# Performance work log

Hardware: AMD Instinct MI355X
Metric: run time of the kernel (lower is better)

## Reference

```python
import jax, jax.numpy as jnp
import numpy as np

D_MODEL = 1024
D_FF = 4096
N_EXPERTS = 4
D_HID = D_MODEL // 2
TOP_K = 2
B, T = 2, 4096


def setup_inputs() -> dict:
    key = jax.random.key(0)
    ks = jax.random.split(key, 10)
    s_in = 1.0 / np.sqrt(D_MODEL)
    s_ff = 1.0 / np.sqrt(D_FF)
    s_h = 1.0 / np.sqrt(D_HID)
    return {
        "x": jax.random.normal(ks[0], (B, T, D_MODEL), jnp.float32),
        # stacked expert FFN params [E, ...]
        "w1": jax.random.normal(ks[1], (N_EXPERTS, D_MODEL, D_FF), jnp.float32) * s_in,
        "b1": jnp.zeros((N_EXPERTS, D_FF), jnp.float32),
        "w2": jax.random.normal(ks[2], (N_EXPERTS, D_FF, D_MODEL), jnp.float32) * s_ff,
        "b2": jnp.zeros((N_EXPERTS, D_MODEL), jnp.float32),
        # router MLP params
        "wr1": jax.random.normal(ks[3], (D_MODEL, D_HID), jnp.float32) * s_in,
        "br1": jnp.zeros((D_HID,), jnp.float32),
        "wr2": jax.random.normal(ks[4], (D_HID, N_EXPERTS), jnp.float32) * s_h,
        "br2": jnp.zeros((N_EXPERTS,), jnp.float32),
    }


def _gelu(x):
    return jax.nn.gelu(x, approximate=False)  # torch nn.GELU default is exact erf


def reference(x, w1, b1, w2, b2, wr1, br1, wr2, br2):
    # Router: 2-layer MLP -> logits [B,T,E]
    h = _gelu(jnp.einsum('btd,dh->bth', x, wr1) + br1)
    logits = jnp.einsum('bth,he->bte', h, wr2) + br2
    # top-k masked softmax over experts
    top_vals, _ = jax.lax.top_k(logits, TOP_K)
    thresh = top_vals[..., -1:]
    masked = jnp.where(logits >= thresh, logits, -jnp.inf)
    gate = jax.nn.softmax(masked, axis=-1)  # [B,T,E], zeros off top-k
    # dense all-experts FFN: hid [B,T,E,d_ff]
    hid = _gelu(jnp.einsum('btd,edf->btef', x, w1) + b1)
    expert_outs = jnp.einsum('btef,efd->bted', hid, w2) + b2  # [B,T,E,d_model]
    out = jnp.einsum('bte,bted->btd', gate, expert_outs)
    return out, gate
```

## Files before the change

kernel.cpp:

```cpp
#include <hip/hip_runtime.h>

#define NTOK 8192
#define DM 1024
#define DF 4096
#define DH 512
#define NE 4
#define SLOTS (NTOK * 2)

typedef unsigned short ushort_t;
typedef short bf16x8 __attribute__((ext_vector_type(8)));
typedef float f32x4 __attribute__((ext_vector_type(4)));

__device__ __forceinline__ unsigned short f2bf(float f) {
    unsigned int u = __float_as_uint(f);
    u += 0x7FFFu + ((u >> 16) & 1u);
    return (unsigned short)(u >> 16);
}
__device__ __forceinline__ float bf2f(unsigned short h) {
    return __uint_as_float(((unsigned int)h) << 16);
}
__device__ __forceinline__ float gelu_exact(float x) {
    return 0.5f * x * (1.0f + erff(x * 0.7071067811865476f));
}
__device__ __forceinline__ float gelu_fast(float x) {
    float u = 1.5957691216057308f * (x + 0.044715f * x * x * x);
    return x / (1.0f + __expf(-u));
}
__device__ __forceinline__ void gload16(const void* g, void* l) {
    __builtin_amdgcn_global_load_lds((__attribute__((address_space(1))) void*)(g),
                                     (__attribute__((address_space(3))) void*)(l), 16, 0, 0);
}
__device__ __forceinline__ int swz(int b) { return b ^ (((b >> 7) & 3) << 4); }
__device__ __forceinline__ int imin(int a, int b) { return a < b ? a : b; }

__global__ __launch_bounds__(256) void k_cast_split(const float* __restrict__ in,
                                                    ushort_t* __restrict__ hi,
                                                    ushort_t* __restrict__ lo, int n4) {
    int i = blockIdx.x * 256 + threadIdx.x;
    if (i >= n4) return;
    float4 v = ((const float4*)in)[i];
    ushort4 h, l;
    h.x = f2bf(v.x); l.x = f2bf(v.x - bf2f(h.x));
    h.y = f2bf(v.y); l.y = f2bf(v.y - bf2f(h.y));
    h.z = f2bf(v.z); l.z = f2bf(v.z - bf2f(h.z));
    h.w = f2bf(v.w); l.w = f2bf(v.w - bf2f(h.w));
    ((ushort4*)hi)[i] = h;
    ((ushort4*)lo)[i] = l;
}

template <bool SPLIT>
__global__ __launch_bounds__(256) void k_tcast(const float* __restrict__ in,
                                               ushort_t* __restrict__ oh,
                                               ushort_t* __restrict__ ol, int K, int N) {
    __shared__ float t[64][65];
    size_t base = (size_t)blockIdx.z * K * N;
    const float* src = in + base;
    int k0 = blockIdx.y * 64, n0 = blockIdx.x * 64;
    int tx = threadIdx.x & 63, ty = threadIdx.x >> 6;
#pragma unroll
    for (int i = 0; i < 16; i++) {
        int r = ty + i * 4;
        t[r][tx] = src[(size_t)(k0 + r) * N + n0 + tx];
    }
    __syncthreads();
#pragma unroll
    for (int i = 0; i < 16; i++) {
        int nn = ty + i * 4;
        float v = t[tx][nn];
        unsigned short hv = f2bf(v);
        size_t o = base + (size_t)(n0 + nn) * K + k0 + tx;
        oh[o] = hv;
        if (SPLIT) ol[o] = f2bf(v - bf2f(hv));
    }
}

template <int MODE>
__global__ __launch_bounds__(256) void k_gemm(
    const ushort_t* __restrict__ A0, const ushort_t* __restrict__ B0,
    const ushort_t* __restrict__ A1, const ushort_t* __restrict__ B1,
    const ushort_t* __restrict__ A2, const ushort_t* __restrict__ B2,
    int K, int N,
    const float* __restrict__ bias, const float* __restrict__ gate,
    const int* __restrict__ idx, const int4* __restrict__ tiles,
    const int* __restrict__ meta,
    float* __restrict__ outF, ushort_t* __restrict__ ghid, float* __restrict__ outA)
{
    int e = 0, rstart = 0, rows = 128, gbase = 0;
    if (MODE != 0) {
        if ((int)blockIdx.y >= meta[0]) return;
        int4 ti = tiles[blockIdx.y];
        e = ti.x; rstart = ti.y; rows = ti.z; gbase = ti.w;
    }
    __shared__ ushort_t lA[4096];
    __shared__ ushort_t lB[4096];
    int row0 = (MODE == 0) ? blockIdx.y * 128 : 0;
    int col0 = blockIdx.x * 128;
    int tid = threadIdx.x, lane = tid & 63, wv = tid >> 6;
    int wr = wv >> 1, wc = wv & 1;
    int r15 = lane & 15, hq = lane >> 4;

    f32x4 z = {0.f, 0.f, 0.f, 0.f};
    f32x4 acc[4][4];
#pragma unroll
    for (int m = 0; m < 4; m++)
#pragma unroll
        for (int n = 0; n < 4; n++) acc[m][n] = z;

    int d0 = tid * 16, d1 = d0 + 4096;
    int u0 = swz(d0), u1 = swz(d1);
    int rA0 = u0 >> 6, ko0 = ((u0 >> 4) & 3) * 8;
    int rA1 = u1 >> 6, ko1 = ((u1 >> 4) & 3) * 8;
    char* ldA0 = (char*)lA + wv * 1024;
    char* ldA1 = (char*)lA + 4096 + wv * 1024;
    char* ldB0 = (char*)lB + wv * 1024;
    char* ldB1 = (char*)lB + 4096 + wv * 1024;

    auto compute = [&]() {
        bf16x8 af[4], bfr[4];
#pragma unroll
        for (int m = 0; m < 4; m++) {
            int u = ((wr * 64 + m * 16 + r15) << 6) + (hq << 4);
            af[m] = *(const bf16x8*)((const char*)lA + swz(u));
        }
#pragma unroll
        for (int n = 0; n < 4; n++) {
            int u = ((wc * 64 + n * 16 + r15) << 6) + (hq << 4);
            bfr[n] = *(const bf16x8*)((const char*)lB + swz(u));
        }
#pragma unroll
        for (int m = 0; m < 4; m++)
#pragma unroll
            for (int n = 0; n < 4; n++)
                acc[m][n] = __builtin_amdgcn_mfma_f32_16x16x32_bf16(af[m], bfr[n], acc[m][n], 0, 0, 0);
    };

    if (MODE == 0) {
#pragma unroll
        for (int p = 0; p < 3; p++) {
            const ushort_t* A = (p == 0) ? A0 : ((p == 1) ? A1 : A2);
            const ushort_t* B = (p == 0) ? B0 : ((p == 1) ? B1 : B2);
            const ushort_t* Ab0 = A + (size_t)(row0 + rA0) * K + ko0;
            const ushort_t* Ab1 = A + (size_t)(row0 + rA1) * K + ko1;
            const ushort_t* Bb0 = B + (size_t)(col0 + rA0) * K + ko0;
            const ushort_t* Bb1 = B + (size_t)(col0 + rA1) * K + ko1;
            for (int kt = 0; kt < K; kt += 32) {
                gload16(Ab0 + kt, ldA0);
                gload16(Ab1 + kt, ldA1);
                gload16(Bb0 + kt, ldB0);
                gload16(Bb1 + kt, ldB1);
                __syncthreads();
                compute();
                __syncthreads();
            }
        }
    } else {
        const ushort_t *Ab0, *Ab1, *Bb0, *Bb1;
        if (MODE == 1) {
            int t0 = idx[e * NTOK + rstart + imin(rA0, rows - 1)];
            int t1 = idx[e * NTOK + rstart + imin(rA1, rows - 1)];
            Ab0 = A0 + (size_t)t0 * K + ko0;
            Ab1 = A0 + (size_t)t1 * K + ko1;
            Bb0 = B0 + ((size_t)e * DF + col0 + rA0) * K + ko0;
            Bb1 = B0 + ((size_t)e * DF + col0 + rA1) * K + ko1;
        } else {
            Ab0 = A0 + (size_t)(gbase + imin(rA0, rows - 1)) * K + ko0;
            Ab1 = A0 + (size_t)(gbase + imin(rA1, rows - 1)) * K + ko1;
            Bb0 = B0 + ((size_t)e * DM + col0 + rA0) * K + ko0;
            Bb1 = B0 + ((size_t)e * DM + col0 + rA1) * K + ko1;
        }
        for (int kt = 0; kt < K; kt += 32) {
            gload16(Ab0 + kt, ldA0);
            gload16(Ab1 + kt, ldA1);
            gload16(Bb0 + kt, ldB0);
            gload16(Bb1 + kt, ldB1);
            __syncthreads();
            compute();
            __syncthreads();
        }
    }

    if (MODE == 0) {
#pragma unroll
        for (int m = 0; m < 4; m++)
#pragma unroll
            for (int q = 0; q < 4; q++) {
                int row = row0 + wr * 64 + m * 16 + hq * 4 + q;
#pragma unroll
                for (int n = 0; n < 4; n++) {
                    int col = col0 + wc * 64 + n * 16 + r15;
                    outF[(size_t)row * N + col] = gelu_exact(acc[m][n][q] + bias[col]);
                }
            }
    } else if (MODE == 1) {
#pragma unroll
        for (int m = 0; m < 4; m++)
#pragma unroll
            for (int q = 0; q < 4; q++) {
                int lr = wr * 64 + m * 16 + hq * 4 + q;
                if (lr < rows) {
                    int token = idx[e * NTOK + rstart + lr];
                    float g = gate[token * 4 + e];
                    size_t rb = (size_t)(gbase + lr) * N;
#pragma unroll
                    for (int n = 0; n < 4; n++) {
                        int col = col0 + wc * 64 + n * 16 + r15;
                        float v = gelu_fast(acc[m][n][q] + bias[(size_t)e * N + col]) * g;
                        ghid[rb + col] = f2bf(v);
                    }
                }
            }
    } else {
#pragma unroll
        for (int m = 0; m < 4; m++)
#pragma unroll
            for (int q = 0; q < 4; q++) {
                int lr = wr * 64 + m * 16 + hq * 4 + q;
                if (lr < rows) {
                    int token = idx[e * NTOK + rstart + lr];
#pragma unroll
                    for (int n = 0; n < 4; n++) {
                        int col = col0 + wc * 64 + n * 16 + r15;
                        atomicAdd(&outA[(size_t)token * N + col], acc[m][n][q]);
                    }
                }
            }
    }
}

__global__ __launch_bounds__(256) void k_gate(const float* __restrict__ h,
                                              const float* __restrict__ wr2,
                                              const float* __restrict__ br2,
                                              float* __restrict__ gate,
                                              int* __restrict__ cnt,
                                              int* __restrict__ idx) {
    int t = blockIdx.x * 4 + (threadIdx.x >> 6);
    int lane = threadIdx.x & 63;
    const float* hr = h + (size_t)t * DH;
    const float4* w4 = (const float4*)wr2;
    float gx = 0.f, gy = 0.f, gz = 0.f, gw = 0.f;
#pragma unroll
    for (int j = 0; j < 8; j++) {
        int k = lane * 8 + j;
        float hv = hr[k];
        float4 w = w4[k];
        gx += hv * w.x; gy += hv * w.y; gz += hv * w.z; gw += hv * w.w;
    }
#pragma unroll
    for (int off = 32; off > 0; off >>= 1) {
        gx += __shfl_xor(gx, off);
        gy += __shfl_xor(gy, off);
        gz += __shfl_xor(gz, off);
        gw += __shfl_xor(gw, off);
    }
    if (lane == 0) {
        float ls[4];
        ls[0] = gx + br2[0]; ls[1] = gy + br2[1]; ls[2] = gz + br2[2]; ls[3] = gw + br2[3];
        int i1 = 0; float m1 = ls[0];
#pragma unroll
        for (int i = 1; i < 4; i++) if (ls[i] > m1) { m1 = ls[i]; i1 = i; }
        int i2 = -1; float m2 = -1e30f;
#pragma unroll
        for (int i = 0; i < 4; i++) if (i != i1 && ls[i] > m2) { m2 = ls[i]; i2 = i; }
        float e0 = (ls[0] >= m2) ? expf(ls[0] - m1) : 0.f;
        float e1 = (ls[1] >= m2) ? expf(ls[1] - m1) : 0.f;
        float e2 = (ls[2] >= m2) ? expf(ls[2] - m1) : 0.f;
        float e3 = (ls[3] >= m2) ? expf(ls[3] - m1) : 0.f;
        float iz = 1.f / (e0 + e1 + e2 + e3);
        float4 g = {e0 * iz, e1 * iz, e2 * iz, e3 * iz};
        ((float4*)gate)[t] = g;
        int s0 = atomicAdd(&cnt[i1], 1);
        idx[i1 * NTOK + s0] = t;
        int s1 = atomicAdd(&cnt[i2], 1);
        idx[i2 * NTOK + s1] = t;
    }
}

__global__ void k_tiles(const int* __restrict__ cnt, int4* __restrict__ tiles,
                        int* __restrict__ meta) {
    if (threadIdx.x != 0 || blockIdx.x != 0) return;
    int base = 0, nt = 0;
    for (int e = 0; e < NE; e++) {
        int c = cnt[e];
        for (int r = 0; r < c; r += 128) {
            int4 ti;
            ti.x = e; ti.y = r; ti.z = (c - r < 128) ? (c - r) : 128; ti.w = base + r;
            tiles[nt++] = ti;
        }
        base += c;
    }
    meta[0] = nt;
}

__global__ __launch_bounds__(256) void k_init_out(const float* __restrict__ gate,
                                                  const float* __restrict__ b2,
                                                  float* __restrict__ out) {
    int i = blockIdx.x * 256 + threadIdx.x;
    int t = i >> 8;
    int c4 = i & 255;
    float4 g = ((const float4*)gate)[t];
    const float4* b = (const float4*)b2;
    float4 v0 = b[c4], v1 = b[256 + c4], v2 = b[512 + c4], v3 = b[768 + c4];
    float4 o;
    o.x = g.x * v0.x + g.y * v1.x + g.z * v2.x + g.w * v3.x;
    o.y = g.x * v0.y + g.y * v1.y + g.z * v2.y + g.w * v3.y;
    o.z = g.x * v0.z + g.y * v1.z + g.z * v2.z + g.w * v3.z;
    o.w = g.x * v0.w + g.y * v1.w + g.z * v2.w + g.w * v3.w;
    ((float4*)out)[i] = o;
}

extern "C" void kernel_launch(void* const* d_in, const int* in_sizes, int n_in,
                              void* d_out, int out_size, void* d_ws, size_t ws_size,
                              hipStream_t stream) {
    const float* x   = (const float*)d_in[0];
    const float* w1  = (const float*)d_in[1];
    const float* b1  = (const float*)d_in[2];
    const float* w2  = (const float*)d_in[3];
    const float* b2  = (const float*)d_in[4];
    const float* wr1 = (const float*)d_in[5];
    const float* br1 = (const float*)d_in[6];
    const float* wr2 = (const float*)d_in[7];
    const float* br2 = (const float*)d_in[8];
    float* out  = (float*)d_out;
    float* gate = out + (size_t)NTOK * DM;

    char* p = (char*)d_ws;
    auto take = [&](size_t bytes) { char* r = p; p += (bytes + 255) & ~(size_t)255; return r; };
    ushort_t* xh    = (ushort_t*)take((size_t)NTOK * DM * 2);
    ushort_t* w1T   = (ushort_t*)take((size_t)NE * DF * DM * 2);
    ushort_t* w2T   = (ushort_t*)take((size_t)NE * DM * DF * 2);
    ushort_t* wr1Th = (ushort_t*)take((size_t)DH * DM * 2);
    ushort_t* wr1Tl = (ushort_t*)take((size_t)DH * DM * 2);
    int*      cnt   = (int*)take(64);
    int*      idx   = (int*)take((size_t)NE * NTOK * 4);
    int4*     tiles = (int4*)take(144 * 16);
    int*      meta  = (int*)take(64);
    char*     region = take((size_t)SLOTS * DF * 2);
    ushort_t* xl    = (ushort_t*)region;
    float*    h     = (float*)(region + (size_t)NTOK * DM * 2);
    ushort_t* ghid  = (ushort_t*)region;

    hipMemsetAsync(cnt, 0, 64, stream);

    k_cast_split<<<NTOK * DM / 4 / 256, 256, 0, stream>>>(x, xh, xl, NTOK * DM / 4);
    k_tcast<false><<<dim3(DF / 64, DM / 64, NE), 256, 0, stream>>>(w1, w1T, nullptr, DM, DF);
    k_tcast<false><<<dim3(DM / 64, DF / 64, NE), 256, 0, stream>>>(w2, w2T, nullptr, DF, DM);
    k_tcast<true ><<<dim3(DH / 64, DM / 64, 1),  256, 0, stream>>>(wr1, wr1Th, wr1Tl, DM, DH);

    k_gemm<0><<<dim3(DH / 128, NTOK / 128), 256, 0, stream>>>(
        xh, wr1Th, xh, wr1Tl, xl, wr1Th, DM, DH, br1,
        nullptr, nullptr, nullptr, nullptr, h, nullptr, nullptr);
    k_gate<<<NTOK / 4, 256, 0, stream>>>(h, wr2, br2, gate, cnt, idx);
    k_tiles<<<1, 64, 0, stream>>>(cnt, tiles, meta);
    k_init_out<<<NTOK * DM / 4 / 256, 256, 0, stream>>>(gate, b2, out);

    k_gemm<1><<<dim3(DF / 128, 132), 256, 0, stream>>>(
        xh, w1T, nullptr, nullptr, nullptr, nullptr, DM, DF, b1,
        gate, idx, tiles, meta, nullptr, ghid, nullptr);
    k_gemm<2><<<dim3(DM / 128, 132), 256, 0, stream>>>(
        ghid, w2T, nullptr, nullptr, nullptr, nullptr, DF, DM, nullptr,
        nullptr, idx, tiles, meta, nullptr, nullptr, out);
}
```

Before: 967.8 us.

## Double-buffer expert GEMMs with 128x256 tiles and XCD-aware block remapping

Splits the router GEMM into its own kernel. The expert GEMMs now use 512-thread blocks with 128x256 output tiles and double-buffered LDS staging, so the next k-slice loads while the current one computes and one barrier per k-step is dropped. It also adds a 1D grid with block-ID remapping across the 8 XCDs for L2 locality. The trade-offs are more LDS per block (48KB) and higher register pressure under launch_bounds(512,4), which could lower occupancy.

```diff
diff --git a/kernel.cpp b/kernel.cpp
--- a/kernel.cpp
+++ b/kernel.cpp
@@ -6,6 +6,7 @@
 #define DH 512
 #define NE 4
 #define SLOTS (NTOK * 2)
+#define NYT_MAX 132
 
 typedef unsigned short ushort_t;
 typedef short bf16x8 __attribute__((ext_vector_type(8)));
@@ -74,27 +75,15 @@
     }
 }
 
-template <int MODE>
-__global__ __launch_bounds__(256) void k_gemm(
+__global__ __launch_bounds__(256) void k_rgemm(
     const ushort_t* __restrict__ A0, const ushort_t* __restrict__ B0,
     const ushort_t* __restrict__ A1, const ushort_t* __restrict__ B1,
     const ushort_t* __restrict__ A2, const ushort_t* __restrict__ B2,
-    int K, int N,
-    const float* __restrict__ bias, const float* __restrict__ gate,
-    const int* __restrict__ idx, const int4* __restrict__ tiles,
-    const int* __restrict__ meta,
-    float* __restrict__ outF, ushort_t* __restrict__ ghid, float* __restrict__ outA)
+    int K, int N, const float* __restrict__ bias, float* __restrict__ outF)
 {
-    int e = 0, rstart = 0, rows = 128, gbase = 0;
-    if (MODE != 0) {
-        if ((int)blockIdx.y >= meta[0]) return;
-        int4 ti = tiles[blockIdx.y];
-        e = ti.x; rstart = ti.y; rows = ti.z; gbase = ti.w;
-    }
     __shared__ ushort_t lA[4096];
     __shared__ ushort_t lB[4096];
-    int row0 = (MODE == 0) ? blockIdx.y * 128 : 0;
-    int col0 = blockIdx.x * 128;
+    int row0 = blockIdx.y * 128, col0 = blockIdx.x * 128;
     int tid = threadIdx.x, lane = tid & 63, wv = tid >> 6;
     int wr = wv >> 1, wc = wv & 1;
     int r15 = lane & 15, hq = lane >> 4;
@@ -115,83 +104,141 @@
     char* ldB0 = (char*)lB + wv * 1024;
     char* ldB1 = (char*)lB + 4096 + wv * 1024;
 
-    auto compute = [&]() {
-        bf16x8 af[4], bfr[4];
-#pragma unroll
-        for (int m = 0; m < 4; m++) {
-            int u = ((wr * 64 + m * 16 + r15) << 6) + (hq << 4);
-            af[m] = *(const bf16x8*)((const char*)lA + swz(u));
-        }
-#pragma unroll
-        for (int n = 0; n < 4; n++) {
-            int u = ((wc * 64 + n * 16 + r15) << 6) + (hq << 4);
-            bfr[n] = *(const bf16x8*)((const char*)lB + swz(u));
-        }
-#pragma unroll
-        for (int m = 0; m < 4; m++)
-#pragma unroll
-            for (int n = 0; n < 4; n++)
-                acc[m][n] = __builtin_amdgcn_mfma_f32_16x16x32_bf16(af[m], bfr[n], acc[m][n], 0, 0, 0);
-    };
-
-    if (MODE == 0) {
-#pragma unroll
-        for (int p = 0; p < 3; p++) {
-            const ushort_t* A = (p == 0) ? A0 : ((p == 1) ? A1 : A2);
-            const ushort_t* B = (p == 0) ? B0 : ((p == 1) ? B1 : B2);
-            const ushort_t* Ab0 = A + (size_t)(row0 + rA0) * K + ko0;
-            const ushort_t* Ab1 = A + (size_t)(row0 + rA1) * K + ko1;
-            const ushort_t* Bb0 = B + (size_t)(col0 + rA0) * K + ko0;
-            const ushort_t* Bb1 = B + (size_t)(col0 + rA1) * K + ko1;
-            for (int kt = 0; kt < K; kt += 32) {
-                gload16(Ab0 + kt, ldA0);
-                gload16(Ab1 + kt, ldA1);
-                gload16(Bb0 + kt, ldB0);
-                gload16(Bb1 + kt, ldB1);
-                __syncthreads();
-                compute();
-                __syncthreads();
-            }
-        }
-    } else {
-        const ushort_t *Ab0, *Ab1, *Bb0, *Bb1;
-        if (MODE == 1) {
-            int t0 = idx[e * NTOK + rstart + imin(rA0, rows - 1)];
-            int t1 = idx[e * NTOK + rstart + imin(rA1, rows - 1)];
-            Ab0 = A0 + (size_t)t0 * K + ko0;
-            Ab1 = A0 + (size_t)t1 * K + ko1;
-            Bb0 = B0 + ((size_t)e * DF + col0 + rA0) * K + ko0;
-            Bb1 = B0 + ((size_t)e * DF + col0 + rA1) * K + ko1;
-        } else {
-            Ab0 = A0 + (size_t)(gbase + imin(rA0, rows - 1)) * K + ko0;
-            Ab1 = A0 + (size_t)(gbase + imin(rA1, rows - 1)) * K + ko1;
-            Bb0 = B0 + ((size_t)e * DM + col0 + rA0) * K + ko0;
-            Bb1 = B0 + ((size_t)e * DM + col0 + rA1) * K + ko1;
-        }
+#pragma unroll
+    for (int p = 0; p < 3; p++) {
+        const ushort_t* A = (p == 0) ? A0 : ((p == 1) ? A1 : A2);
+        const ushort_t* B = (p == 0) ? B0 : ((p == 1) ? B1 : B2);
+        const ushort_t* Ab0 = A + (size_t)(row0 + rA0) * K + ko0;
+        const ushort_t* Ab1 = A + (size_t)(row0 + rA1) * K + ko1;
+        const ushort_t* Bb0 = B + (size_t)(col0 + rA0) * K + ko0;
+        const ushort_t* Bb1 = B + (size_t)(col0 + rA1) * K + ko1;
         for (int kt = 0; kt < K; kt += 32) {
             gload16(Ab0 + kt, ldA0);
             gload16(Ab1 + kt, ldA1);
             gload16(Bb0 + kt, ldB0);
             gload16(Bb1 + kt, ldB1);
             __syncthreads();
-            compute();
+            bf16x8 af[4], bfr[4];
+#pragma unroll
+            for (int m = 0; m < 4; m++) {
+                int u = ((wr * 64 + m * 16 + r15) << 6) + (hq << 4);
+                af[m] = *(const bf16x8*)((const char*)lA + swz(u));
+            }
+#pragma unroll
+            for (int n = 0; n < 4; n++) {
+                int u = ((wc * 64 + n * 16 + r15) << 6) + (hq << 4);
+                bfr[n] = *(const bf16x8*)((const char*)lB + swz(u));
+            }
+#pragma unroll
+            for (int m = 0; m < 4; m++)
+#pragma unroll
+                for (int n = 0; n < 4; n++)
+                    acc[m][n] = __builtin_amdgcn_mfma_f32_16x16x32_bf16(af[m], bfr[n], acc[m][n], 0, 0, 0);
             __syncthreads();
         }
     }
-
-    if (MODE == 0) {
+#pragma unroll
+    for (int m = 0; m < 4; m++)
+#pragma unroll
+        for (int q = 0; q < 4; q++) {
+            int row = row0 + wr * 64 + m * 16 + hq * 4 + q;
+#pragma unroll
+            for (int n = 0; n < 4; n++) {
+                int col = col0 + wc * 64 + n * 16 + r15;
+                outF[(size_t)row * N + col] = gelu_exact(acc[m][n][q] + bias[col]);
+            }
+        }
+}
+
+template <int MODE>
+__global__ __launch_bounds__(512, 4) void k_egemm(
+    const ushort_t* __restrict__ A0, const ushort_t* __restrict__ B0,
+    const float* __restrict__ bias, const float* __restrict__ gate,
+    const int* __restrict__ idx, const int4* __restrict__ tiles,
+    const int* __restrict__ meta,
+    ushort_t* __restrict__ ghid, float* __restrict__ outA)
+{
+    constexpr int K = (MODE == 1) ? DM : DF;
+    constexpr int NFULL = (MODE == 1) ? DF : DM;
+    constexpr int NXT = NFULL / 256;
+    constexpr int nwg = NXT * NYT_MAX;
+    constexpr int q8 = nwg / 8;
+
+    int bid = blockIdx.x;
+    int wgid = (bid & 7) * q8 + (bid >> 3);
+    int xt = wgid / NYT_MAX, yt = wgid % NYT_MAX;
+    if (yt >= meta[0]) return;
+    int4 ti = tiles[yt];
+    int e = ti.x, rstart = ti.y, rows = ti.z, gbase = ti.w;
+    int col0 = xt * 256;
+
+    __shared__ ushort_t lA[2][4096];
+    __shared__ ushort_t lB[2][8192];
+    int tid = threadIdx.x, lane = tid & 63, wv = tid >> 6;
+    int wr = wv >> 2, wc = wv & 3;
+    int r15 = lane & 15, hq = lane >> 4;
+
+    f32x4 z = {0.f, 0.f, 0.f, 0.f};
+    f32x4 acc[4][4];
+#pragma unroll
+    for (int m = 0; m < 4; m++)
+#pragma unroll
+        for (int n = 0; n < 4; n++) acc[m][n] = z;
+
+    int u = swz(tid * 16);
+    int rA = u >> 6;
+    int ko = ((u >> 4) & 3) * 8;
+    const ushort_t *Ab, *Bb0, *Bb1;
+    if (MODE == 1) {
+        int tok = idx[e * NTOK + rstart + imin(rA, rows - 1)];
+        Ab = A0 + (size_t)tok * K + ko;
+    } else {
+        Ab = A0 + (size_t)(gbase + imin(rA, rows - 1)) * K + ko;
+    }
+    Bb0 = B0 + ((size_t)e * NFULL + col0 + rA) * K + ko;
+    Bb1 = B0 + ((size_t)e * NFULL + col0 + 128 + rA) * K + ko;
+
+    char* dstA = (char*)&lA[0][0];
+    char* dstB = (char*)&lB[0][0];
+
+    auto stage = [&](int b, int kt) {
+        gload16(Ab + kt, dstA + b * 8192 + wv * 1024);
+        gload16(Bb0 + kt, dstB + b * 16384 + wv * 1024);
+        gload16(Bb1 + kt, dstB + b * 16384 + 8192 + wv * 1024);
+    };
+    auto compute = [&](int b) {
+        const char* pa = (const char*)&lA[b][0];
+        const char* pb = (const char*)&lB[b][0];
+        bf16x8 af[4], bfr[4];
+#pragma unroll
+        for (int m = 0; m < 4; m++) {
+            int ub = ((wr * 64 + m * 16 + r15) << 6) + (hq << 4);
+            af[m] = *(const bf16x8*)(pa + swz(ub));
+        }
+#pragma unroll
+        for (int n = 0; n < 4; n++) {
+            int ub = ((wc * 64 + n * 16 + r15) << 6) + (hq << 4);
+            bfr[n] = *(const bf16x8*)(pb + swz(ub));
+        }
 #pragma unroll
         for (int m = 0; m < 4; m++)
 #pragma unroll
-            for (int q = 0; q < 4; q++) {
-                int row = row0 + wr * 64 + m * 16 + hq * 4 + q;
-#pragma unroll
-                for (int n = 0; n < 4; n++) {
-                    int col = col0 + wc * 64 + n * 16 + r15;
-                    outF[(size_t)row * N + col] = gelu_exact(acc[m][n][q] + bias[col]);
-                }
-            }
-    } else if (MODE == 1) {
+            for (int n = 0; n < 4; n++)
+                acc[m][n] = __builtin_amdgcn_mfma_f32_16x16x32_bf16(af[m], bfr[n], acc[m][n], 0, 0, 0);
+    };
+
+    stage(0, 0);
+    __syncthreads();
+    int cur = 0;
+    for (int kt = 32; kt < K; kt += 32) {
+        stage(cur ^ 1, kt);
+        compute(cur);
+        __syncthreads();
+        cur ^= 1;
+    }
+    compute(cur);
+
+    if (MODE == 1) {
 #pragma unroll
         for (int m = 0; m < 4; m++)
 #pragma unroll
@@ -200,11 +247,11 @@
                 if (lr < rows) {
                     int token = idx[e * NTOK + rstart + lr];
                     float g = gate[token * 4 + e];
-                    size_t rb = (size_t)(gbase + lr) * N;
+                    size_t rb = (size_t)(gbase + lr) * NFULL;
 #pragma unroll
                     for (int n = 0; n < 4; n++) {
                         int col = col0 + wc * 64 + n * 16 + r15;
-                        float v = gelu_fast(acc[m][n][q] + bias[(size_t)e * N + col]) * g;
+                        float v = gelu_fast(acc[m][n][q] + bias[(size_t)e * NFULL + col]) * g;
                         ghid[rb + col] = f2bf(v);
                     }
                 }
@@ -220,7 +267,7 @@
 #pragma unroll
                     for (int n = 0; n < 4; n++) {
                         int col = col0 + wc * 64 + n * 16 + r15;
-                        atomicAdd(&outA[(size_t)token * N + col], acc[m][n][q]);
+                        atomicAdd(&outA[(size_t)token * NFULL + col], acc[m][n][q]);
                     }
                 }
             }
@@ -346,17 +393,14 @@
     k_tcast<false><<<dim3(DM / 64, DF / 64, NE), 256, 0, stream>>>(w2, w2T, nullptr, DF, DM);
     k_tcast<true ><<<dim3(DH / 64, DM / 64, 1),  256, 0, stream>>>(wr1, wr1Th, wr1Tl, DM, DH);
 
-    k_gemm<0><<<dim3(DH / 128, NTOK / 128), 256, 0, stream>>>(
-        xh, wr1Th, xh, wr1Tl, xl, wr1Th, DM, DH, br1,
-        nullptr, nullptr, nullptr, nullptr, h, nullptr, nullptr);
+    k_rgemm<<<dim3(DH / 128, NTOK / 128), 256, 0, stream>>>(
+        xh, wr1Th, xh, wr1Tl, xl, wr1Th, DM, DH, br1, h);
     k_gate<<<NTOK / 4, 256, 0, stream>>>(h, wr2, br2, gate, cnt, idx);
     k_tiles<<<1, 64, 0, stream>>>(cnt, tiles, meta);
     k_init_out<<<NTOK * DM / 4 / 256, 256, 0, stream>>>(gate, b2, out);
 
-    k_gemm<1><<<dim3(DF / 128, 132), 256, 0, stream>>>(
-        xh, w1T, nullptr, nullptr, nullptr, nullptr, DM, DF, b1,
-        gate, idx, tiles, meta, nullptr, ghid, nullptr);
-    k_gemm<2><<<dim3(DM / 128, 132), 256, 0, stream>>>(
-        ghid, w2T, nullptr, nullptr, nullptr, nullptr, DF, DM, nullptr,
-        nullptr, idx, tiles, meta, nullptr, nullptr, out);
-}
+    k_egemm<1><<<(DF / 256) * NYT_MAX, 512, 0, stream>>>(
+        xh, w1T, b1, gate, idx, tiles, meta, ghid, nullptr);
+    k_egemm<2><<<(DM / 256) * NYT_MAX, 512, 0, stream>>>(
+        ghid, w2T, nullptr, gate, idx, tiles, meta, nullptr, out);
+}
```

Result: no change. 949.0 us (-1.9%).
